# Kernel optimization log

Hardware: AMD Instinct MI355X
Metric: run time of the kernel (lower is better)

The kernel has to match this reference:

```python
import jax, jax.numpy as jnp
import numpy as np

T, H, E, I, K = 1024, 2048, 32, 1024, 2  # tokens, hidden, experts, intermediate (per rank), top_k


def setup_inputs() -> dict:
    key = jax.random.key(0)
    k0, k1, k2, k3 = jax.random.split(key, 4)
    s = 0.02  # weight init scale
    return {
        "hidden_states": jax.random.normal(k0, (T, H), jnp.float32),
        "w_qkv": jax.random.normal(k1, (3 * E, H), jnp.float32) * s,   # router query_key_value weight
        "w1": jax.random.normal(k2, (E, 2 * I, H), jnp.float32) * s,   # gate/up projection per expert
        "w2": jax.random.normal(k3, (E, H, I), jnp.float32) * s,       # down projection per expert
    }


def _router_logits(x, w_qkv):
    # ParallelAttention_router: per-token attention over the expert axis.
    mix = x @ w_qkv.T                      # [T, 3E]
    q, k, v = jnp.split(mix, 3, axis=-1)   # each [T, E]
    q = q.astype(jnp.float32)
    k = k.astype(jnp.float32)
    v = v.astype(jnp.float32)
    # attn[t, e, f] = softmax_f(q[t, e] * k[t, f])
    attn = jax.nn.softmax(q[:, :, None] * k[:, None, :], axis=-1)  # [T, E, E]
    return jnp.einsum('tef,tf->te', attn, v)                        # [T, E]


def reference(hidden_states, w_qkv, w1, w2):
    n_tok = hidden_states.shape[0]
    logits = _router_logits(hidden_states, w_qkv)                   # [T, E]
    top_logits, topk_ids = jax.lax.top_k(logits, K)                 # [T, K]
    topk_w = jax.nn.softmax(top_logits.astype(jnp.float32), axis=-1)  # renormalize=False -> plain softmax over top-k
    # Dense combine weights: zero for non-selected experts (honors top-k sparsity in math).
    combine = jnp.zeros((n_tok, E), jnp.float32).at[
        jnp.arange(n_tok)[:, None], topk_ids].add(topk_w)           # [T, E]
    # Expert MLP: SiLU-gated FFN (fused_experts contract: w1 -> [gate; up], w2 -> down).
    gate_up = jnp.einsum('th,eih->tei', hidden_states, w1)          # [T, E, 2I]
    gate, up = jnp.split(gate_up, 2, axis=-1)                       # each [T, E, I]
    h = jax.nn.silu(gate) * up * combine[:, :, None]                # fold combine weight in early
    out = jnp.einsum('tei,ehi->th', h, w2)                          # [T, H]
    return out.astype(hidden_states.dtype)
```

## Files before the change

kernel.cpp:

```cpp
#include <hip/hip_runtime.h>
#include <hip/hip_bf16.h>
#include <math.h>

#define TT 1024
#define HH 2048
#define EE 32
#define II 1024
#define BK 64
#define SA 72
#define TS (128 * SA)
#define KSP 32
#define MB 64

typedef __attribute__((ext_vector_type(8))) short bf16x8;
typedef __attribute__((ext_vector_type(8))) unsigned short ushort8;
typedef __attribute__((ext_vector_type(4))) float f32x4;

__device__ __forceinline__ unsigned short f2b(float f) {
    union { float f; unsigned u; } c; c.f = f;
    unsigned r = c.u + 0x7FFFu + ((c.u >> 16) & 1u);
    return (unsigned short)(r >> 16);
}
__device__ __forceinline__ float b2f(unsigned short u) {
    union { unsigned u; float f; } c; c.u = ((unsigned)u) << 16;
    return c.f;
}
__device__ __forceinline__ unsigned cvtpk(float lo, float hi) {
    unsigned r;
    asm("v_cvt_pk_bf16_f32 %0, %1, %2" : "=v"(r) : "v"(lo), "v"(hi));
    return r;
}
__device__ __forceinline__ ushort8 pack8(float4 a, float4 b) {
    union { unsigned u[4]; ushort8 s; } cv;
    cv.u[0] = cvtpk(a.x, a.y); cv.u[1] = cvtpk(a.z, a.w);
    cv.u[2] = cvtpk(b.x, b.y); cv.u[3] = cvtpk(b.z, b.w);
    return cv.s;
}

__global__ __launch_bounds__(256) void k_mix(const float* __restrict__ x,
                                             const float* __restrict__ wqkv,
                                             float* __restrict__ mixp) {
    __shared__ float xs[MB][68];
    __shared__ float ws_[96][68];
    const int tm0 = blockIdx.x * MB;
    const int k0 = blockIdx.y * 64;
    const int tid = threadIdx.x;
#pragma unroll
    for (int q = 0; q < 4; ++q) {
        int p = tid + q * 256;
        int row = p >> 4, c4 = (p & 15) * 4;
        *(float4*)&xs[row][c4] = *(const float4*)(x + (size_t)(tm0 + row) * HH + k0 + c4);
    }
#pragma unroll
    for (int q = 0; q < 6; ++q) {
        int p = tid + q * 256;
        int row = p >> 4, c4 = (p & 15) * 4;
        *(float4*)&ws_[row][c4] = *(const float4*)(wqkv + (size_t)row * HH + k0 + c4);
    }
    __syncthreads();
    const int tg = tid >> 4, cg = tid & 15;
    float acc[4][6];
#pragma unroll
    for (int i = 0; i < 4; ++i)
#pragma unroll
        for (int c = 0; c < 6; ++c) acc[i][c] = 0.f;
    for (int k = 0; k < 64; k += 4) {
        float4 xv[4], wv[6];
#pragma unroll
        for (int i = 0; i < 4; ++i) xv[i] = *(const float4*)&xs[tg * 4 + i][k];
#pragma unroll
        for (int c = 0; c < 6; ++c) wv[c] = *(const float4*)&ws_[cg * 6 + c][k];
#pragma unroll
        for (int i = 0; i < 4; ++i)
#pragma unroll
            for (int c = 0; c < 6; ++c)
                acc[i][c] += xv[i].x * wv[c].x + xv[i].y * wv[c].y +
                             xv[i].z * wv[c].z + xv[i].w * wv[c].w;
    }
    float* dst = mixp + ((size_t)blockIdx.y * TT + tm0) * 96;
#pragma unroll
    for (int i = 0; i < 4; ++i)
#pragma unroll
        for (int c = 0; c < 6; ++c)
            dst[(tg * 4 + i) * 96 + cg * 6 + c] = acc[i][c];
}

__global__ void k_router_attn(const float* __restrict__ mixp,
                              int* __restrict__ cnt,
                              int* __restrict__ tok_list,
                              float* __restrict__ wgt_list) {
    const int t = blockIdx.x;
    __shared__ float mrow[96];
    __shared__ float lg[EE];
    const int tid = threadIdx.x;
    if (tid < 96) {
        float s = 0.f;
        for (int sp = 0; sp < KSP; ++sp)
            s += mixp[((size_t)sp * TT + t) * 96 + tid];
        mrow[tid] = s;
    }
    __syncthreads();
    if (tid < EE) {
        float q = mrow[tid];
        float m = -1e30f;
        for (int f = 0; f < EE; ++f) m = fmaxf(m, q * mrow[32 + f]);
        float s = 0.f, a = 0.f;
        for (int f = 0; f < EE; ++f) {
            float ex = expf(q * mrow[32 + f] - m);
            s += ex;
            a += ex * mrow[64 + f];
        }
        lg[tid] = a / s;
    }
    __syncthreads();
    if (tid == 0) {
        int b0 = 0; float v0 = lg[0];
        for (int e2 = 1; e2 < EE; ++e2)
            if (lg[e2] > v0) { v0 = lg[e2]; b0 = e2; }
        int b1 = -1; float v1 = -1e30f;
        for (int e2 = 0; e2 < EE; ++e2)
            if (e2 != b0 && lg[e2] > v1) { v1 = lg[e2]; b1 = e2; }
        float ex = expf(v1 - v0);
        float w0 = 1.f / (1.f + ex);
        float w1 = ex / (1.f + ex);
        int p0 = atomicAdd(&cnt[b0], 1);
        tok_list[b0 * TT + p0] = t * 2 + 0;
        wgt_list[b0 * TT + p0] = w0;
        int p1 = atomicAdd(&cnt[b1], 1);
        tok_list[b1 * TT + p1] = t * 2 + 1;
        wgt_list[b1 * TT + p1] = w1;
    }
}

__global__ __launch_bounds__(256, 2) void k_gemm1(
    const float* __restrict__ x, const float* __restrict__ w1,
    const int* __restrict__ cnt, const int* __restrict__ tok_list,
    unsigned short* __restrict__ gu) {
    const int e = blockIdx.y;
    const int M = cnt[e];
    const int m0 = blockIdx.z * 128;
    if (m0 >= M) return;
    const int n0 = blockIdx.x * 128;

    __shared__ __align__(16) unsigned short As[2 * TS];
    __shared__ __align__(16) unsigned short Bs[2 * TS];
    __shared__ int ts[128];

    const int tid = threadIdx.x;
    if (tid < 128) {
        int mr = m0 + tid;
        ts[tid] = (mr < M) ? tok_list[e * TT + mr] : -1;
    }
    __syncthreads();

    const float* w1e = w1 + (size_t)e * (2 * II) * HH;
    const int wid = tid >> 6;
    const int lane = tid & 63;
    const int wm = wid >> 1, wn = wid & 1;
    const int fr = lane & 15;
    const int kg = lane >> 4;
    const int srow = tid >> 3;
    const int sc8 = (tid & 7) * 8;

    f32x4 acc[4][4];
#pragma unroll
    for (int i = 0; i < 4; ++i)
#pragma unroll
        for (int j = 0; j < 4; ++j) acc[i][j] = (f32x4){0.f, 0.f, 0.f, 0.f};

    float4 pa[8], pb[8];
    const float4 f4z = {0.f, 0.f, 0.f, 0.f};

#define G1_LOAD(kk)                                                              \
    do {                                                                         \
        const int kkv_ = (kk);                                                   \
        _Pragma("unroll")                                                        \
        for (int q = 0; q < 4; ++q) {                                            \
            int row = srow + q * 32;                                             \
            int entry = ts[row];                                                 \
            if (entry >= 0) {                                                    \
                const float* gpa_ = x + (size_t)(entry >> 1) * HH + kkv_ + sc8;  \
                pa[2 * q] = ((const float4*)gpa_)[0];                            \
                pa[2 * q + 1] = ((const float4*)gpa_)[1];                        \
            } else { pa[2 * q] = f4z; pa[2 * q + 1] = f4z; }                     \
            const float* gpb_ = w1e + (size_t)(n0 + row) * HH + kkv_ + sc8;      \
            pb[2 * q] = ((const float4*)gpb_)[0];                                \
            pb[2 * q + 1] = ((const float4*)gpb_)[1];                            \
        }                                                                        \
    } while (0)

#define G1_CVT(buf)                                                              \
    do {                                                                         \
        unsigned short* Ad = As + (buf)*TS;                                      \
        unsigned short* Bd = Bs + (buf)*TS;                                      \
        _Pragma("unroll")                                                        \
        for (int q = 0; q < 4; ++q) {                                            \
            int row = srow + q * 32;                                             \
            *(ushort8*)&Ad[row * SA + sc8] = pack8(pa[2 * q], pa[2 * q + 1]);    \
            *(ushort8*)&Bd[row * SA + sc8] = pack8(pb[2 * q], pb[2 * q + 1]);    \
        }                                                                        \
    } while (0)

    const int NS = HH / BK;
    G1_LOAD(0);
    G1_CVT(0);
    G1_LOAD(BK);
    __syncthreads();

    for (int s = 0; s < NS; ++s) {
        const int cur = s & 1;
        if (s + 1 < NS) {
            G1_CVT(cur ^ 1);
            if (s + 2 < NS) G1_LOAD((s + 2) * BK);
        }
        const unsigned short* Ar = As + cur * TS;
        const unsigned short* Br = Bs + cur * TS;
#pragma unroll
        for (int kh = 0; kh < 2; ++kh) {
            const int kb = kh * 32 + kg * 8;
            bf16x8 a[4], b[4];
#pragma unroll
            for (int i = 0; i < 4; ++i)
                a[i] = *(const bf16x8*)&Ar[(wm * 64 + i * 16 + fr) * SA + kb];
#pragma unroll
            for (int j = 0; j < 4; ++j)
                b[j] = *(const bf16x8*)&Br[(wn * 64 + j * 16 + fr) * SA + kb];
#pragma unroll
            for (int i = 0; i < 4; ++i)
#pragma unroll
                for (int j = 0; j < 4; ++j)
                    acc[i][j] = __builtin_amdgcn_mfma_f32_16x16x32_bf16(a[i], b[j], acc[i][j], 0, 0, 0);
        }
        __syncthreads();
    }
#undef G1_LOAD
#undef G1_CVT

#pragma unroll
    for (int mi = 0; mi < 4; ++mi) {
#pragma unroll
        for (int reg = 0; reg < 4; ++reg) {
            int m = wm * 64 + mi * 16 + kg * 4 + reg;
            int entry = ts[m];
            if (entry < 0) continue;
            unsigned short* dst = gu + (size_t)entry * (2 * II) + n0 + wn * 64;
#pragma unroll
            for (int ni = 0; ni < 4; ++ni)
                dst[ni * 16 + fr] = f2b(acc[mi][ni][reg]);
        }
    }
}

__global__ __launch_bounds__(256, 2) void k_gemm2(
    const unsigned short* __restrict__ gu, const float* __restrict__ w2,
    const int* __restrict__ cnt, const int* __restrict__ tok_list,
    const float* __restrict__ wgt_list, float* __restrict__ po) {
    const int e = blockIdx.y;
    const int M = cnt[e];
    const int m0 = blockIdx.z * 128;
    if (m0 >= M) return;
    const int n0 = blockIdx.x * 128;

    __shared__ __align__(16) unsigned short As[2 * TS];
    __shared__ __align__(16) unsigned short Bs[2 * TS];
    __shared__ int ts[128];
    __shared__ float tw[128];

    const int tid = threadIdx.x;
    if (tid < 128) {
        int mr = m0 + tid;
        if (mr < M) {
            ts[tid] = tok_list[e * TT + mr];
            tw[tid] = wgt_list[e * TT + mr];
        } else { ts[tid] = -1; tw[tid] = 0.f; }
    }
    __syncthreads();

    const float* w2e = w2 + (size_t)e * HH * II;
    const int wid = tid >> 6;
    const int lane = tid & 63;
    const int wm = wid >> 1, wn = wid & 1;
    const int fr = lane & 15;
    const int kg = lane >> 4;
    const int srow = tid >> 3;
    const int sc8 = (tid & 7) * 8;

    f32x4 acc[4][4];
#pragma unroll
    for (int i = 0; i < 4; ++i)
#pragma unroll
        for (int j = 0; j < 4; ++j) acc[i][j] = (f32x4){0.f, 0.f, 0.f, 0.f};

    ushort8 pg[4], pu[4];
    float4 pb[8];
    const ushort8 u8z = {0, 0, 0, 0, 0, 0, 0, 0};

#define G2_LOAD(kk)                                                                  \
    do {                                                                             \
        const int kkv_ = (kk);                                                       \
        _Pragma("unroll")                                                            \
        for (int q = 0; q < 4; ++q) {                                                \
            int row = srow + q * 32;                                                 \
            int entry = ts[row];                                                     \
            if (entry >= 0) {                                                        \
                pg[q] = *(const ushort8*)(gu + (size_t)entry * (2 * II) + kkv_ + sc8);      \
                pu[q] = *(const ushort8*)(gu + (size_t)entry * (2 * II) + II + kkv_ + sc8); \
            } else { pg[q] = u8z; pu[q] = u8z; }                                     \
            const float* gpb_ = w2e + (size_t)(n0 + row) * II + kkv_ + sc8;          \
            pb[2 * q] = ((const float4*)gpb_)[0];                                    \
            pb[2 * q + 1] = ((const float4*)gpb_)[1];                                \
        }                                                                            \
    } while (0)

#define G2_CVT(buf)                                                                  \
    do {                                                                             \
        unsigned short* Ad = As + (buf)*TS;                                          \
        unsigned short* Bd = Bs + (buf)*TS;                                          \
        _Pragma("unroll")                                                            \
        for (int q = 0; q < 4; ++q) {                                                \
            int row = srow + q * 32;                                                 \
            float w = tw[row];                                                       \
            float s0[8];                                                             \
            _Pragma("unroll")                                                        \
            for (int j = 0; j < 8; ++j) {                                            \
                float g = b2f((unsigned short)pg[q][j]);                             \
                float u = b2f((unsigned short)pu[q][j]);                             \
                s0[j] = (g / (1.f + __expf(-g))) * u * w;                            \
            }                                                                        \
            float4 lo = make_float4(s0[0], s0[1], s0[2], s0[3]);                     \
            float4 hi = make_float4(s0[4], s0[5], s0[6], s0[7]);                     \
            *(ushort8*)&Ad[row * SA + sc8] = pack8(lo, hi);                          \
            *(ushort8*)&Bd[row * SA + sc8] = pack8(pb[2 * q], pb[2 * q + 1]);        \
        }                                                                            \
    } while (0)

    const int NS = II / BK;
    G2_LOAD(0);
    G2_CVT(0);
    G2_LOAD(BK);
    __syncthreads();

    for (int s = 0; s < NS; ++s) {
        const int cur = s & 1;
        if (s + 1 < NS) {
            G2_CVT(cur ^ 1);
            if (s + 2 < NS) G2_LOAD((s + 2) * BK);
        }
        const unsigned short* Ar = As + cur * TS;
        const unsigned short* Br = Bs + cur * TS;
#pragma unroll
        for (int kh = 0; kh < 2; ++kh) {
            const int kb = kh * 32 + kg * 8;
            bf16x8 a[4], b[4];
#pragma unroll
            for (int i = 0; i < 4; ++i)
                a[i] = *(const bf16x8*)&Ar[(wm * 64 + i * 16 + fr) * SA + kb];
#pragma unroll
            for (int j = 0; j < 4; ++j)
                b[j] = *(const bf16x8*)&Br[(wn * 64 + j * 16 + fr) * SA + kb];
#pragma unroll
            for (int i = 0; i < 4; ++i)
#pragma unroll
                for (int j = 0; j < 4; ++j)
                    acc[i][j] = __builtin_amdgcn_mfma_f32_16x16x32_bf16(a[i], b[j], acc[i][j], 0, 0, 0);
        }
        __syncthreads();
    }
#undef G2_LOAD
#undef G2_CVT

#pragma unroll
    for (int mi = 0; mi < 4; ++mi) {
#pragma unroll
        for (int reg = 0; reg < 4; ++reg) {
            int m = wm * 64 + mi * 16 + kg * 4 + reg;
            int entry = ts[m];
            if (entry < 0) continue;
            float* op = po + (size_t)entry * HH + n0 + wn * 64;
#pragma unroll
            for (int ni = 0; ni < 4; ++ni)
                op[ni * 16 + fr] = acc[mi][ni][reg];
        }
    }
}

__global__ __launch_bounds__(256) void k_combine(const float* __restrict__ po,
                                                 float* __restrict__ out) {
    int i = blockIdx.x * 256 + threadIdx.x;
    int t = i / (HH / 4);
    int c = i % (HH / 4);
    float4 a = ((const float4*)(po + (size_t)(2 * t) * HH))[c];
    float4 b = ((const float4*)(po + (size_t)(2 * t + 1) * HH))[c];
    float4 r = make_float4(a.x + b.x, a.y + b.y, a.z + b.z, a.w + b.w);
    ((float4*)(out + (size_t)t * HH))[c] = r;
}

extern "C" void kernel_launch(void* const* d_in, const int* in_sizes, int n_in,
                              void* d_out, int out_size, void* d_ws, size_t ws_size,
                              hipStream_t stream) {
    const float* x    = (const float*)d_in[0];
    const float* wqkv = (const float*)d_in[1];
    const float* w1   = (const float*)d_in[2];
    const float* w2   = (const float*)d_in[3];
    float* out = (float*)d_out;

    char* ws = (char*)d_ws;
    float* mixp           = (float*)(ws);
    float* wgt_list       = (float*)(ws + 12582912);
    int*   tok_list       = (int*)  (ws + 12713984);
    int*   cnt            = (int*)  (ws + 12845056);
    unsigned short* gu    = (unsigned short*)(ws + 12845184);
    float* po             = (float*)(ws + 21233792);

    (void)hipMemsetAsync(cnt, 0, 128, stream);

    k_mix<<<dim3(TT / MB, KSP), 256, 0, stream>>>(x, wqkv, mixp);
    k_router_attn<<<TT, 128, 0, stream>>>(mixp, cnt, tok_list, wgt_list);
    k_gemm1<<<dim3(2 * II / 128, EE, 8), 256, 0, stream>>>(x, w1, cnt, tok_list, gu);
    k_gemm2<<<dim3(HH / 128, EE, 8), 256, 0, stream>>>(gu, w2, cnt, tok_list, wgt_list, po);
    k_combine<<<TT * HH / 4 / 256, 256, 0, stream>>>(po, out);
}
```

Baseline: 249.5 us.

## Deepen GEMM prefetch pipeline with paired weight-tile loads and lighter barriers

Both expert GEMM kernels now load the fp32 weight tile for two consecutive K-steps at once and prefetch activations three steps ahead. Conversion into shared memory moves after the MFMA compute and reuses the buffer that was just consumed. The full __syncthreads is replaced by a barrier that waits only on LDS counters, so outstanding global loads stay in flight across it. The aim is to hide more global-memory latency behind compute. The cost is many more live registers for the doubled weight buffer, which risks spills or lower occupancy.

```diff
diff --git a/kernel.cpp b/kernel.cpp
--- a/kernel.cpp
+++ b/kernel.cpp
@@ -15,6 +15,11 @@
 typedef __attribute__((ext_vector_type(8))) short bf16x8;
 typedef __attribute__((ext_vector_type(8))) unsigned short ushort8;
 typedef __attribute__((ext_vector_type(4))) float f32x4;
+
+#define SOFT_BARRIER() do { \
+    asm volatile("s_waitcnt lgkmcnt(0)" ::: "memory"); \
+    __builtin_amdgcn_s_barrier(); \
+} while (0)
 
 __device__ __forceinline__ unsigned short f2b(float f) {
     union { float f; unsigned u; } c; c.f = f;
@@ -168,10 +173,11 @@
 #pragma unroll
         for (int j = 0; j < 4; ++j) acc[i][j] = (f32x4){0.f, 0.f, 0.f, 0.f};
 
-    float4 pa[8], pb[8];
+    float4 pa[8];
+    float4 pbb[16];
     const float4 f4z = {0.f, 0.f, 0.f, 0.f};
 
-#define G1_LOAD(kk)                                                              \
+#define G1_LOADA(kk)                                                             \
     do {                                                                         \
         const int kkv_ = (kk);                                                   \
         _Pragma("unroll")                                                        \
@@ -183,13 +189,24 @@
                 pa[2 * q] = ((const float4*)gpa_)[0];                            \
                 pa[2 * q + 1] = ((const float4*)gpa_)[1];                        \
             } else { pa[2 * q] = f4z; pa[2 * q + 1] = f4z; }                     \
+        }                                                                        \
+    } while (0)
+
+#define G1_LOADB2(kk)                                                            \
+    do {                                                                         \
+        const int kkv_ = (kk);                                                   \
+        _Pragma("unroll")                                                        \
+        for (int q = 0; q < 4; ++q) {                                            \
+            int row = srow + q * 32;                                             \
             const float* gpb_ = w1e + (size_t)(n0 + row) * HH + kkv_ + sc8;      \
-            pb[2 * q] = ((const float4*)gpb_)[0];                                \
-            pb[2 * q + 1] = ((const float4*)gpb_)[1];                            \
+            pbb[4 * q + 0] = ((const float4*)gpb_)[0];                           \
+            pbb[4 * q + 1] = ((const float4*)gpb_)[1];                           \
+            pbb[4 * q + 2] = ((const float4*)(gpb_ + 64))[0];                    \
+            pbb[4 * q + 3] = ((const float4*)(gpb_ + 64))[1];                    \
         }                                                                        \
     } while (0)
 
-#define G1_CVT(buf)                                                              \
+#define G1_CVT(buf, h)                                                           \
     do {                                                                         \
         unsigned short* Ad = As + (buf)*TS;                                      \
         unsigned short* Bd = Bs + (buf)*TS;                                      \
@@ -197,22 +214,23 @@
         for (int q = 0; q < 4; ++q) {                                            \
             int row = srow + q * 32;                                             \
             *(ushort8*)&Ad[row * SA + sc8] = pack8(pa[2 * q], pa[2 * q + 1]);    \
-            *(ushort8*)&Bd[row * SA + sc8] = pack8(pb[2 * q], pb[2 * q + 1]);    \
+            *(ushort8*)&Bd[row * SA + sc8] =                                     \
+                pack8(pbb[4 * q + (h)*2], pbb[4 * q + (h)*2 + 1]);               \
         }                                                                        \
     } while (0)
 
     const int NS = HH / BK;
-    G1_LOAD(0);
-    G1_CVT(0);
-    G1_LOAD(BK);
-    __syncthreads();
+    G1_LOADB2(0);
+    G1_LOADA(0);
+    G1_CVT(0, 0);
+    G1_LOADA(BK);
+    G1_CVT(1, 1);
+    G1_LOADB2(2 * BK);
+    G1_LOADA(2 * BK);
+    SOFT_BARRIER();
 
     for (int s = 0; s < NS; ++s) {
         const int cur = s & 1;
-        if (s + 1 < NS) {
-            G1_CVT(cur ^ 1);
-            if (s + 2 < NS) G1_LOAD((s + 2) * BK);
-        }
         const unsigned short* Ar = As + cur * TS;
         const unsigned short* Br = Bs + cur * TS;
 #pragma unroll
@@ -231,9 +249,17 @@
                 for (int j = 0; j < 4; ++j)
                     acc[i][j] = __builtin_amdgcn_mfma_f32_16x16x32_bf16(a[i], b[j], acc[i][j], 0, 0, 0);
         }
-        __syncthreads();
-    }
-#undef G1_LOAD
+        SOFT_BARRIER();
+        if (s + 2 < NS) {
+            G1_CVT(cur, cur);
+            if (s + 3 < NS) {
+                G1_LOADA((s + 3) * BK);
+                if (cur == 1) G1_LOADB2((s + 3) * BK);
+            }
+        }
+    }
+#undef G1_LOADA
+#undef G1_LOADB2
 #undef G1_CVT
 
 #pragma unroll
@@ -292,10 +318,10 @@
         for (int j = 0; j < 4; ++j) acc[i][j] = (f32x4){0.f, 0.f, 0.f, 0.f};
 
     ushort8 pg[4], pu[4];
-    float4 pb[8];
+    float4 pbb[16];
     const ushort8 u8z = {0, 0, 0, 0, 0, 0, 0, 0};
 
-#define G2_LOAD(kk)                                                                  \
+#define G2_LOADA(kk)                                                                 \
     do {                                                                             \
         const int kkv_ = (kk);                                                       \
         _Pragma("unroll")                                                            \
@@ -306,13 +332,24 @@
                 pg[q] = *(const ushort8*)(gu + (size_t)entry * (2 * II) + kkv_ + sc8);      \
                 pu[q] = *(const ushort8*)(gu + (size_t)entry * (2 * II) + II + kkv_ + sc8); \
             } else { pg[q] = u8z; pu[q] = u8z; }                                     \
+        }                                                                            \
+    } while (0)
+
+#define G2_LOADB2(kk)                                                                \
+    do {                                                                             \
+        const int kkv_ = (kk);                                                       \
+        _Pragma("unroll")                                                            \
+        for (int q = 0; q < 4; ++q) {                                                \
+            int row = srow + q * 32;                                                 \
             const float* gpb_ = w2e + (size_t)(n0 + row) * II + kkv_ + sc8;          \
-            pb[2 * q] = ((const float4*)gpb_)[0];                                    \
-            pb[2 * q + 1] = ((const float4*)gpb_)[1];                                \
+            pbb[4 * q + 0] = ((const float4*)gpb_)[0];                               \
+            pbb[4 * q + 1] = ((const float4*)gpb_)[1];                               \
+            pbb[4 * q + 2] = ((const float4*)(gpb_ + 64))[0];                        \
+            pbb[4 * q + 3] = ((const float4*)(gpb_ + 64))[1];                        \
         }                                                                            \
     } while (0)
 
-#define G2_CVT(buf)                                                                  \
+#define G2_CVT(buf, h)                                                               \
     do {                                                                             \
         unsigned short* Ad = As + (buf)*TS;                                          \
         unsigned short* Bd = Bs + (buf)*TS;                                          \
@@ -330,22 +367,23 @@
             float4 lo = make_float4(s0[0], s0[1], s0[2], s0[3]);                     \
             float4 hi = make_float4(s0[4], s0[5], s0[6], s0[7]);                     \
             *(ushort8*)&Ad[row * SA + sc8] = pack8(lo, hi);                          \
-            *(ushort8*)&Bd[row * SA + sc8] = pack8(pb[2 * q], pb[2 * q + 1]);        \
+            *(ushort8*)&Bd[row * SA + sc8] =                                         \
+                pack8(pbb[4 * q + (h)*2], pbb[4 * q + (h)*2 + 1]);                   \
         }                                                                            \
     } while (0)
 
     const int NS = II / BK;
-    G2_LOAD(0);
-    G2_CVT(0);
-    G2_LOAD(BK);
-    __syncthreads();
+    G2_LOADB2(0);
+    G2_LOADA(0);
+    G2_CVT(0, 0);
+    G2_LOADA(BK);
+    G2_CVT(1, 1);
+    G2_LOADB2(2 * BK);
+    G2_LOADA(2 * BK);
+    SOFT_BARRIER();
 
     for (int s = 0; s < NS; ++s) {
         const int cur = s & 1;
-        if (s + 1 < NS) {
-            G2_CVT(cur ^ 1);
-            if (s + 2 < NS) G2_LOAD((s + 2) * BK);
-        }
         const unsigned short* Ar = As + cur * TS;
         const unsigned short* Br = Bs + cur * TS;
 #pragma unroll
@@ -364,9 +402,17 @@
                 for (int j = 0; j < 4; ++j)
                     acc[i][j] = __builtin_amdgcn_mfma_f32_16x16x32_bf16(a[i], b[j], acc[i][j], 0, 0, 0);
         }
-        __syncthreads();
-    }
-#undef G2_LOAD
+        SOFT_BARRIER();
+        if (s + 2 < NS) {
+            G2_CVT(cur, cur);
+            if (s + 3 < NS) {
+                G2_LOADA((s + 3) * BK);
+                if (cur == 1) G2_LOADB2((s + 3) * BK);
+            }
+        }
+    }
+#undef G2_LOADA
+#undef G2_LOADB2
 #undef G2_CVT
 
 #pragma unroll
```

After: 451.0 us. 80.8% more time.

## Fuse SiLU-gating into gemm1 epilogue, pre-convert x to bf16, single-buffer LDS

Applied to the files above, without the earlier changes.

A new kernel converts x to bf16 once, so gemm1 gathers half-size rows and no longer converts A tiles. Gemm1 now tiles 64 gate columns together with the matching 64 up columns, then applies SiLU, the up product and the routing weight in its epilogue via an LDS exchange. It writes a compact bf16 activation tensor that gemm2 reads directly, cutting gemm2's A reads in half and removing its elementwise work. Both GEMMs drop LDS double-buffering and use two barriers per k-step, which frees shared memory but loses the overlap between tile conversion and MFMA.

```diff
diff --git a/kernel.cpp b/kernel.cpp
--- a/kernel.cpp
+++ b/kernel.cpp
@@ -35,6 +35,14 @@
     cv.u[0] = cvtpk(a.x, a.y); cv.u[1] = cvtpk(a.z, a.w);
     cv.u[2] = cvtpk(b.x, b.y); cv.u[3] = cvtpk(b.z, b.w);
     return cv.s;
+}
+
+__global__ __launch_bounds__(256) void k_cvtx(const float* __restrict__ x,
+                                              unsigned short* __restrict__ xb) {
+    int i = blockIdx.x * 256 + threadIdx.x;
+    const float4* s = (const float4*)(x + (size_t)i * 8);
+    float4 v0 = s[0], v1 = s[1];
+    *(ushort8*)(xb + (size_t)i * 8) = pack8(v0, v1);
 }
 
 __global__ __launch_bounds__(256) void k_mix(const float* __restrict__ x,
@@ -133,23 +141,27 @@
 }
 
 __global__ __launch_bounds__(256, 2) void k_gemm1(
-    const float* __restrict__ x, const float* __restrict__ w1,
+    const unsigned short* __restrict__ xb, const float* __restrict__ w1,
     const int* __restrict__ cnt, const int* __restrict__ tok_list,
-    unsigned short* __restrict__ gu) {
+    const float* __restrict__ wgt_list, unsigned short* __restrict__ act) {
     const int e = blockIdx.y;
     const int M = cnt[e];
     const int m0 = blockIdx.z * 128;
     if (m0 >= M) return;
-    const int n0 = blockIdx.x * 128;
-
-    __shared__ __align__(16) unsigned short As[2 * TS];
-    __shared__ __align__(16) unsigned short Bs[2 * TS];
+    const int i0 = blockIdx.x * 64;
+
+    __shared__ __align__(16) unsigned short As[TS];
+    __shared__ __align__(16) unsigned short Bs[TS];
     __shared__ int ts[128];
+    __shared__ float tw[128];
 
     const int tid = threadIdx.x;
     if (tid < 128) {
         int mr = m0 + tid;
-        ts[tid] = (mr < M) ? tok_list[e * TT + mr] : -1;
+        if (mr < M) {
+            ts[tid] = tok_list[e * TT + mr];
+            tw[tid] = wgt_list[e * TT + mr];
+        } else { ts[tid] = -1; tw[tid] = 0.f; }
     }
     __syncthreads();
 
@@ -168,8 +180,9 @@
 #pragma unroll
         for (int j = 0; j < 4; ++j) acc[i][j] = (f32x4){0.f, 0.f, 0.f, 0.f};
 
-    float4 pa[8], pb[8];
-    const float4 f4z = {0.f, 0.f, 0.f, 0.f};
+    ushort8 pa8[4];
+    float4 pb[8];
+    const ushort8 u8z = {0, 0, 0, 0, 0, 0, 0, 0};
 
 #define G1_LOAD(kk)                                                              \
     do {                                                                         \
@@ -178,101 +191,105 @@
         for (int q = 0; q < 4; ++q) {                                            \
             int row = srow + q * 32;                                             \
             int entry = ts[row];                                                 \
-            if (entry >= 0) {                                                    \
-                const float* gpa_ = x + (size_t)(entry >> 1) * HH + kkv_ + sc8;  \
-                pa[2 * q] = ((const float4*)gpa_)[0];                            \
-                pa[2 * q + 1] = ((const float4*)gpa_)[1];                        \
-            } else { pa[2 * q] = f4z; pa[2 * q + 1] = f4z; }                     \
-            const float* gpb_ = w1e + (size_t)(n0 + row) * HH + kkv_ + sc8;      \
+            pa8[q] = (entry >= 0)                                                \
+                ? *(const ushort8*)(xb + (size_t)(entry >> 1) * HH + kkv_ + sc8) \
+                : u8z;                                                           \
+            int brow = (row < 64) ? (i0 + row) : (II + i0 + row - 64);           \
+            const float* gpb_ = w1e + (size_t)brow * HH + kkv_ + sc8;            \
             pb[2 * q] = ((const float4*)gpb_)[0];                                \
             pb[2 * q + 1] = ((const float4*)gpb_)[1];                            \
         }                                                                        \
     } while (0)
 
-#define G1_CVT(buf)                                                              \
+#define G1_CVT()                                                                 \
     do {                                                                         \
-        unsigned short* Ad = As + (buf)*TS;                                      \
-        unsigned short* Bd = Bs + (buf)*TS;                                      \
         _Pragma("unroll")                                                        \
         for (int q = 0; q < 4; ++q) {                                            \
             int row = srow + q * 32;                                             \
-            *(ushort8*)&Ad[row * SA + sc8] = pack8(pa[2 * q], pa[2 * q + 1]);    \
-            *(ushort8*)&Bd[row * SA + sc8] = pack8(pb[2 * q], pb[2 * q + 1]);    \
+            *(ushort8*)&As[row * SA + sc8] = pa8[q];                             \
+            *(ushort8*)&Bs[row * SA + sc8] = pack8(pb[2 * q], pb[2 * q + 1]);    \
         }                                                                        \
     } while (0)
 
     const int NS = HH / BK;
     G1_LOAD(0);
-    G1_CVT(0);
-    G1_LOAD(BK);
-    __syncthreads();
-
     for (int s = 0; s < NS; ++s) {
-        const int cur = s & 1;
-        if (s + 1 < NS) {
-            G1_CVT(cur ^ 1);
-            if (s + 2 < NS) G1_LOAD((s + 2) * BK);
-        }
-        const unsigned short* Ar = As + cur * TS;
-        const unsigned short* Br = Bs + cur * TS;
+        __syncthreads();
+        G1_CVT();
+        __syncthreads();
+        if (s + 1 < NS) G1_LOAD((s + 1) * BK);
 #pragma unroll
         for (int kh = 0; kh < 2; ++kh) {
             const int kb = kh * 32 + kg * 8;
             bf16x8 a[4], b[4];
 #pragma unroll
             for (int i = 0; i < 4; ++i)
-                a[i] = *(const bf16x8*)&Ar[(wm * 64 + i * 16 + fr) * SA + kb];
+                a[i] = *(const bf16x8*)&As[(wm * 64 + i * 16 + fr) * SA + kb];
 #pragma unroll
             for (int j = 0; j < 4; ++j)
-                b[j] = *(const bf16x8*)&Br[(wn * 64 + j * 16 + fr) * SA + kb];
+                b[j] = *(const bf16x8*)&Bs[(wn * 64 + j * 16 + fr) * SA + kb];
 #pragma unroll
             for (int i = 0; i < 4; ++i)
 #pragma unroll
                 for (int j = 0; j < 4; ++j)
                     acc[i][j] = __builtin_amdgcn_mfma_f32_16x16x32_bf16(a[i], b[j], acc[i][j], 0, 0, 0);
         }
-        __syncthreads();
     }
 #undef G1_LOAD
 #undef G1_CVT
 
-#pragma unroll
-    for (int mi = 0; mi < 4; ++mi) {
-#pragma unroll
-        for (int reg = 0; reg < 4; ++reg) {
-            int m = wm * 64 + mi * 16 + kg * 4 + reg;
-            int entry = ts[m];
-            if (entry < 0) continue;
-            unsigned short* dst = gu + (size_t)entry * (2 * II) + n0 + wn * 64;
-#pragma unroll
-            for (int ni = 0; ni < 4; ++ni)
-                dst[ni * 16 + fr] = f2b(acc[mi][ni][reg]);
-        }
+    unsigned short* upls = As;
+    __syncthreads();
+    if (wn == 1) {
+#pragma unroll
+        for (int mi = 0; mi < 4; ++mi)
+#pragma unroll
+            for (int reg = 0; reg < 4; ++reg) {
+                int mrow = wm * 64 + mi * 16 + kg * 4 + reg;
+#pragma unroll
+                for (int ni = 0; ni < 4; ++ni)
+                    upls[mrow * 64 + ni * 16 + fr] = f2b(acc[mi][ni][reg]);
+            }
+    }
+    __syncthreads();
+    if (wn == 0) {
+#pragma unroll
+        for (int mi = 0; mi < 4; ++mi)
+#pragma unroll
+            for (int reg = 0; reg < 4; ++reg) {
+                int mrow = wm * 64 + mi * 16 + kg * 4 + reg;
+                int entry = ts[mrow];
+                if (entry < 0) continue;
+                float w = tw[mrow];
+                unsigned short* dst = act + (size_t)entry * II + i0;
+#pragma unroll
+                for (int ni = 0; ni < 4; ++ni) {
+                    float g = acc[mi][ni][reg];
+                    float u = b2f(upls[mrow * 64 + ni * 16 + fr]);
+                    dst[ni * 16 + fr] = f2b((g / (1.f + __expf(-g))) * u * w);
+                }
+            }
     }
 }
 
 __global__ __launch_bounds__(256, 2) void k_gemm2(
-    const unsigned short* __restrict__ gu, const float* __restrict__ w2,
+    const unsigned short* __restrict__ act, const float* __restrict__ w2,
     const int* __restrict__ cnt, const int* __restrict__ tok_list,
-    const float* __restrict__ wgt_list, float* __restrict__ po) {
+    float* __restrict__ po) {
     const int e = blockIdx.y;
     const int M = cnt[e];
     const int m0 = blockIdx.z * 128;
     if (m0 >= M) return;
     const int n0 = blockIdx.x * 128;
 
-    __shared__ __align__(16) unsigned short As[2 * TS];
-    __shared__ __align__(16) unsigned short Bs[2 * TS];
+    __shared__ __align__(16) unsigned short As[TS];
+    __shared__ __align__(16) unsigned short Bs[TS];
     __shared__ int ts[128];
-    __shared__ float tw[128];
 
     const int tid = threadIdx.x;
     if (tid < 128) {
         int mr = m0 + tid;
-        if (mr < M) {
-            ts[tid] = tok_list[e * TT + mr];
-            tw[tid] = wgt_list[e * TT + mr];
-        } else { ts[tid] = -1; tw[tid] = 0.f; }
+        ts[tid] = (mr < M) ? tok_list[e * TT + mr] : -1;
     }
     __syncthreads();
 
@@ -291,80 +308,59 @@
 #pragma unroll
         for (int j = 0; j < 4; ++j) acc[i][j] = (f32x4){0.f, 0.f, 0.f, 0.f};
 
-    ushort8 pg[4], pu[4];
+    ushort8 pa8[4];
     float4 pb[8];
     const ushort8 u8z = {0, 0, 0, 0, 0, 0, 0, 0};
 
-#define G2_LOAD(kk)                                                                  \
-    do {                                                                             \
-        const int kkv_ = (kk);                                                       \
-        _Pragma("unroll")                                                            \
-        for (int q = 0; q < 4; ++q) {                                                \
-            int row = srow + q * 32;                                                 \
-            int entry = ts[row];                                                     \
-            if (entry >= 0) {                                                        \
-                pg[q] = *(const ushort8*)(gu + (size_t)entry * (2 * II) + kkv_ + sc8);      \
-                pu[q] = *(const ushort8*)(gu + (size_t)entry * (2 * II) + II + kkv_ + sc8); \
-            } else { pg[q] = u8z; pu[q] = u8z; }                                     \
-            const float* gpb_ = w2e + (size_t)(n0 + row) * II + kkv_ + sc8;          \
-            pb[2 * q] = ((const float4*)gpb_)[0];                                    \
-            pb[2 * q + 1] = ((const float4*)gpb_)[1];                                \
-        }                                                                            \
+#define G2_LOAD(kk)                                                              \
+    do {                                                                         \
+        const int kkv_ = (kk);                                                   \
+        _Pragma("unroll")                                                        \
+        for (int q = 0; q < 4; ++q) {                                            \
+            int row = srow + q * 32;                                             \
+            int entry = ts[row];                                                 \
+            pa8[q] = (entry >= 0)                                                \
+                ? *(const ushort8*)(act + (size_t)entry * II + kkv_ + sc8)       \
+                : u8z;                                                           \
+            const float* gpb_ = w2e + (size_t)(n0 + row) * II + kkv_ + sc8;      \
+            pb[2 * q] = ((const float4*)gpb_)[0];                                \
+            pb[2 * q + 1] = ((const float4*)gpb_)[1];                            \
+        }                                                                        \
     } while (0)
 
-#define G2_CVT(buf)                                                                  \
-    do {                                                                             \
-        unsigned short* Ad = As + (buf)*TS;                                          \
-        unsigned short* Bd = Bs + (buf)*TS;                                          \
-        _Pragma("unroll")                                                            \
-        for (int q = 0; q < 4; ++q) {                                                \
-            int row = srow + q * 32;                                                 \
-            float w = tw[row];                                                       \
-            float s0[8];                                                             \
-            _Pragma("unroll")                                                        \
-            for (int j = 0; j < 8; ++j) {                                            \
-                float g = b2f((unsigned short)pg[q][j]);                             \
-                float u = b2f((unsigned short)pu[q][j]);                             \
-                s0[j] = (g / (1.f + __expf(-g))) * u * w;                            \
-            }                                                                        \
-            float4 lo = make_float4(s0[0], s0[1], s0[2], s0[3]);                     \
-            float4 hi = make_float4(s0[4], s0[5], s0[6], s0[7]);                     \
-            *(ushort8*)&Ad[row * SA + sc8] = pack8(lo, hi);                          \
-            *(ushort8*)&Bd[row * SA + sc8] = pack8(pb[2 * q], pb[2 * q + 1]);        \
-        }                                                                            \
+#define G2_CVT()                                                                 \
+    do {                                                                         \
+        _Pragma("unroll")                                                        \
+        for (int q = 0; q < 4; ++q) {                                            \
+            int row = srow + q * 32;                                             \
+            *(ushort8*)&As[row * SA + sc8] = pa8[q];                             \
+            *(ushort8*)&Bs[row * SA + sc8] = pack8(pb[2 * q], pb[2 * q + 1]);    \
+        }                                                                        \
     } while (0)
 
     const int NS = II / BK;
     G2_LOAD(0);
-    G2_CVT(0);
-    G2_LOAD(BK);
-    __syncthreads();
-
     for (int s = 0; s < NS; ++s) {
-        const int cur = s & 1;
-        if (s + 1 < NS) {
-            G2_CVT(cur ^ 1);
-            if (s + 2 < NS) G2_LOAD((s + 2) * BK);
-        }
-        const unsigned short* Ar = As + cur * TS;
-        const unsigned short* Br = Bs + cur * TS;
+        __syncthreads();
+        G2_CVT();
+        __syncthreads();
+        if (s + 1 < NS) G2_LOAD((s + 1) * BK);
 #pragma unroll
         for (int kh = 0; kh < 2; ++kh) {
             const int kb = kh * 32 + kg * 8;
             bf16x8 a[4], b[4];
 #pragma unroll
             for (int i = 0; i < 4; ++i)
-                a[i] = *(const bf16x8*)&Ar[(wm * 64 + i * 16 + fr) * SA + kb];
+                a[i] = *(const bf16x8*)&As[(wm * 64 + i * 16 + fr) * SA + kb];
 #pragma unroll
             for (int j = 0; j < 4; ++j)
-                b[j] = *(const bf16x8*)&Br[(wn * 64 + j * 16 + fr) * SA + kb];
+                b[j] = *(const bf16x8*)&Bs[(wn * 64 + j * 16 + fr) * SA + kb];
 #pragma unroll
             for (int i = 0; i < 4; ++i)
 #pragma unroll
                 for (int j = 0; j < 4; ++j)
                     acc[i][j] = __builtin_amdgcn_mfma_f32_16x16x32_bf16(a[i], b[j], acc[i][j], 0, 0, 0);
         }
-        __syncthreads();
     }
 #undef G2_LOAD
 #undef G2_CVT
@@ -409,14 +405,16 @@
     float* wgt_list       = (float*)(ws + 12582912);
     int*   tok_list       = (int*)  (ws + 12713984);
     int*   cnt            = (int*)  (ws + 12845056);
-    unsigned short* gu    = (unsigned short*)(ws + 12845184);
+    unsigned short* xb    = (unsigned short*)(ws + 12845184);
+    unsigned short* act   = (unsigned short*)(ws + 17039488);
     float* po             = (float*)(ws + 21233792);
 
     (void)hipMemsetAsync(cnt, 0, 128, stream);
 
+    k_cvtx<<<TT * HH / 8 / 256, 256, 0, stream>>>(x, xb);
     k_mix<<<dim3(TT / MB, KSP), 256, 0, stream>>>(x, wqkv, mixp);
     k_router_attn<<<TT, 128, 0, stream>>>(mixp, cnt, tok_list, wgt_list);
-    k_gemm1<<<dim3(2 * II / 128, EE, 8), 256, 0, stream>>>(x, w1, cnt, tok_list, gu);
-    k_gemm2<<<dim3(HH / 128, EE, 8), 256, 0, stream>>>(gu, w2, cnt, tok_list, wgt_list, po);
+    k_gemm1<<<dim3(II / 64, EE, 8), 256, 0, stream>>>(xb, w1, cnt, tok_list, wgt_list, act);
+    k_gemm2<<<dim3(HH / 128, EE, 8), 256, 0, stream>>>(act, w2, cnt, tok_list, po);
     k_combine<<<TT * HH / 4 / 256, 256, 0, stream>>>(po, out);
 }
```

Result: slower. 257.9 us (+3.4%).
